# Kernel tuning notes

Hardware: AMD Instinct MI355X
Metric: run time of the kernel (lower is better)

The kernel has to match this reference:

```python
import jax, jax.numpy as jnp
import numpy as np

B, T, V = 8, 2048, 1024


def setup_inputs() -> dict:
    key = jax.random.key(0)
    k1, k2, k3, k4, k5 = jax.random.split(key, 5)
    idx = jax.random.randint(k1, (B, T), 0, V)
    # nn.Embedding(length, 1) weight, std=0.02
    v = 0.02 * jax.random.normal(k2, (T, 1), dtype=jnp.float32)
    # nn.Linear(V, V, bias=False) weights (torch layout: out x in), std=0.02
    Wk = 0.02 * jax.random.normal(k3, (V, V), dtype=jnp.float32)
    Wq = 0.02 * jax.random.normal(k4, (V, V), dtype=jnp.float32)
    Wv = 0.02 * jax.random.normal(k5, (V, V), dtype=jnp.float32)
    return {"idx": idx, "v": v, "Wk": Wk, "Wq": Wq, "Wv": Wv}


def reference(idx, v, Wk, Wq, Wv):
    Tn = v.shape[0]
    Vn = Wk.shape[0]
    # one-hot token embedding [B, T, V]
    e = jax.nn.one_hot(idx, Vn, dtype=jnp.float32)
    # relative positions, clipped at 0; pos_embd[i, j] = v[i-j] for i >= j else 0
    pos = jnp.arange(Tn)
    rel = jnp.clip(pos[:, None] - pos[None, :], 0)
    pos_embd = jnp.tril(v[rel, 0])  # [T, T]
    # layer_one = pos_embd @ e  -> [B, T, V]
    layer_one = jnp.einsum('ts,bsv->btv', pos_embd, e)
    K = layer_one @ Wk.T           # Linear: x @ W^T
    Q = e @ Wq.T
    attention = jnp.einsum('btv,bsv->bts', Q, K)  # [B, T, T]
    causal = jnp.tril(jnp.ones((Tn, Tn), dtype=bool))
    masked_attention = jnp.where(causal, attention, 0.0)
    output = jnp.einsum('bts,bsv->btv', masked_attention, e @ Wv.T)
    logits = output + 0.001
    return logits
```

## Files before the change

### kernel.cpp

```cpp
#include <hip/hip_runtime.h>
#include <stdint.h>

#define T_DIM 2048
#define V_DIM 1024
#define B_DIM 8
#define NT 16

typedef unsigned int u32;
typedef unsigned short u16;
typedef __attribute__((ext_vector_type(8))) short s16x8;
typedef __attribute__((ext_vector_type(4))) float f32x4;

__device__ __forceinline__ u16 f2bf(float x) {
  u32 u = __builtin_bit_cast(u32, x);
  u = u + 0x7FFFu + ((u >> 16) & 1u);
  return (u16)(u >> 16);
}

#define GLD16(gp, lp) __builtin_amdgcn_global_load_lds( \
    (const __attribute__((address_space(1))) u32*)(gp), \
    (__attribute__((address_space(3))) u32*)(lp), 16, 0, 0)

template<int MODE, bool F32OUT>
__global__ void __launch_bounds__(256, 2)
gemm_bt(const u16* __restrict__ A, int lda, long long batchA,
        const u16* __restrict__ Bt, int ldb, long long batchB,
        void* __restrict__ Cv, int ldc, long long batchC,
        int K, float bias)
{
  int bn, bm, bz;
  if (MODE == 0) {
    bn = blockIdx.x; bm = blockIdx.y; bz = blockIdx.z;
  } else if (MODE == 1) {
    int lam = blockIdx.x;
    int tau = lam >> 3; bz = lam & 7;
    int b = NT - 1, off = 0;
    while (tau >= off + (NT - b)) { off += NT - b; b--; }
    bn = b; bm = b + (tau - off);
  } else {
    int lam = blockIdx.x;
    bm = (NT - 1) - (lam >> 6);
    bn = (lam >> 3) & 7;
    bz = lam & 7;
  }
  const u16* Ab = A + (long long)bz * batchA;
  const u16* Bb = Bt + (long long)bz * batchB;
  int m0 = bm * 128, n0 = bn * 128;
  int kmax = K;
  if (MODE == 1) { int kl = (bn + 1) * 128; kmax = kl < K ? kl : K; }
  if (MODE == 2) { int kl = (bm + 1) * 128; kmax = kl < K ? kl : K; }

  __shared__ u16 As[128 * 64];
  __shared__ u16 Bs[128 * 64];

  int tid = threadIdx.x;
  int lane = tid & 63;
  int wid = tid >> 6;
  int wm = wid >> 1, wn = wid & 1;

  f32x4 acc[4][4] = {};

  int r0 = tid >> 3;
  int gcol = (((tid & 7) - r0) & 7) * 8;
  const u16* ga = Ab + (long long)(m0 + r0) * lda + gcol;
  const u16* gb = Bb + (long long)(n0 + r0) * ldb + gcol;
  u16* la = As + tid * 8;
  u16* lb = Bs + tid * 8;
  long long lda32 = (long long)32 * lda;
  long long ldb32 = (long long)32 * ldb;

  int rm = lane & 15;
  int q = lane >> 4;

  for (int k0 = 0; k0 < kmax; k0 += 64) {
#pragma unroll
    for (int i = 0; i < 4; i++)
      GLD16(ga + k0 + i * lda32, la + i * 2048);
#pragma unroll
    for (int i = 0; i < 4; i++)
      GLD16(gb + k0 + i * ldb32, lb + i * 2048);
    __syncthreads();
#pragma unroll
    for (int ks = 0; ks < 2; ks++) {
      s16x8 af[4], bfv[4];
#pragma unroll
      for (int mi = 0; mi < 4; mi++) {
        int row = wm * 64 + mi * 16 + rm;
        int p = ((ks * 4 + q) + row) & 7;
        af[mi] = *(const s16x8*)&As[row * 64 + p * 8];
      }
#pragma unroll
      for (int ni = 0; ni < 4; ni++) {
        int row = wn * 64 + ni * 16 + rm;
        int p = ((ks * 4 + q) + row) & 7;
        bfv[ni] = *(const s16x8*)&Bs[row * 64 + p * 8];
      }
#pragma unroll
      for (int mi = 0; mi < 4; mi++)
#pragma unroll
        for (int ni = 0; ni < 4; ni++)
          acc[mi][ni] = __builtin_amdgcn_mfma_f32_16x16x32_bf16(
              af[mi], bfv[ni], acc[mi][ni], 0, 0, 0);
    }
    __syncthreads();
  }

  int col = lane & 15;
  int rq = (lane >> 4) * 4;
#pragma unroll
  for (int mi = 0; mi < 4; mi++) {
#pragma unroll
    for (int ni = 0; ni < 4; ni++) {
      int lr = wm * 64 + mi * 16 + rq;
      int lc = wn * 64 + ni * 16 + col;
#pragma unroll
      for (int rr = 0; rr < 4; rr++) {
        float val = acc[mi][ni][rr];
        if (MODE == 1 && (n0 + lc) > (m0 + lr + rr)) val = 0.f;
        long long off = (long long)(m0 + lr + rr) * ldc + (n0 + lc);
        if (F32OUT) {
          float* C = (float*)Cv + (long long)bz * batchC;
          C[off] = val + bias;
        } else {
          u16* C = (u16*)Cv + (long long)bz * batchC;
          C[off] = f2bf(val);
        }
      }
    }
  }
}

__global__ void prep_weights(const float* __restrict__ Wq, u16* __restrict__ WqT,
                             const float* __restrict__ Wk, u16* __restrict__ WkT,
                             const float* __restrict__ Wv, u16* __restrict__ Wvb)
{
  int z = blockIdx.z;
  if (z == 2) {
    int bx = blockIdx.y * 32 + blockIdx.x;
    int i = bx * 1024 + threadIdx.y * 32 + threadIdx.x;
#pragma unroll
    for (int k = 0; k < 4; k++) Wvb[i + k * 256] = f2bf(Wv[i + k * 256]);
    return;
  }
  const float* src = z ? Wk : Wq;
  u16* dst = z ? WkT : WqT;
  __shared__ float tile[32][33];
  int x0 = blockIdx.x * 32, y0 = blockIdx.y * 32;
  int tx = threadIdx.x, ty = threadIdx.y;
#pragma unroll
  for (int k = 0; k < 4; k++)
    tile[ty + k * 8][tx] = src[(long long)(y0 + ty + k * 8) * V_DIM + x0 + tx];
  __syncthreads();
#pragma unroll
  for (int k = 0; k < 4; k++)
    dst[(long long)(x0 + ty + k * 8) * V_DIM + y0 + tx] = f2bf(tile[tx][ty + k * 8]);
}

__global__ void build_p(const float* __restrict__ v, u16* __restrict__ P)
{
  int gid = blockIdx.x * 256 + threadIdx.x;
  int e0 = gid * 8;
  int s = e0 >> 11, u0 = e0 & 2047;
  s16x8 o;
#pragma unroll
  for (int k = 0; k < 8; k++) {
    int u = u0 + k;
    o[k] = (short)((u <= s) ? f2bf(v[s - u]) : (u16)0);
  }
  *(s16x8*)&P[e0] = o;
}

__global__ void __launch_bounds__(256)
gather_gy(const int* __restrict__ idx, const u16* __restrict__ Mb,
          const u16* __restrict__ Wvb, u16* __restrict__ G,
          u16* __restrict__ Yt, int b0)
{
  int bx = blockIdx.x, z = blockIdx.y;
  const int* idxrow = idx + (long long)(b0 + z) * T_DIM;
  __shared__ u16 Row[V_DIM];
  int tid = threadIdx.x;
  const u32* src;
  u16* dst;
  if (bx < T_DIM) {
    src = (const u32*)(Mb + (long long)idxrow[bx] * V_DIM);
    dst = G + ((long long)z * T_DIM + bx) * T_DIM;
  } else {
    src = (const u32*)(Wvb + (long long)(bx - T_DIM) * V_DIM);
    dst = Yt + ((long long)z * V_DIM + (bx - T_DIM)) * T_DIM;
  }
  u32* dstl = (u32*)Row;
  dstl[tid] = src[tid];
  dstl[tid + 256] = src[tid + 256];
  __syncthreads();
  int s0 = tid * 8;
  int4 i0 = *(const int4*)&idxrow[s0];
  int4 i1 = *(const int4*)&idxrow[s0 + 4];
  s16x8 o;
  o[0] = (short)Row[i0.x]; o[1] = (short)Row[i0.y];
  o[2] = (short)Row[i0.z]; o[3] = (short)Row[i0.w];
  o[4] = (short)Row[i1.x]; o[5] = (short)Row[i1.y];
  o[6] = (short)Row[i1.z]; o[7] = (short)Row[i1.w];
  *(s16x8*)&dst[s0] = o;
}

extern "C" void kernel_launch(void* const* d_in, const int* in_sizes, int n_in,
                              void* d_out, int out_size, void* d_ws, size_t ws_size,
                              hipStream_t stream)
{
  const int*   idx = (const int*)d_in[0];
  const float* v   = (const float*)d_in[1];
  const float* Wk  = (const float*)d_in[2];
  const float* Wq  = (const float*)d_in[3];
  const float* Wv  = (const float*)d_in[4];
  float* out = (float*)d_out;

  char* p = (char*)d_ws;
  const size_t SZ_VV = (size_t)V_DIM * V_DIM * 2;
  const size_t SZ_TT = (size_t)T_DIM * T_DIM * 2;
  const size_t SZ_VT = (size_t)V_DIM * T_DIM * 2;
  u16* WqT = (u16*)p; p += SZ_VV;
  u16* WkT = (u16*)p; p += SZ_VV;
  u16* Wvb = (u16*)p; p += SZ_VV;
  u16* Mb  = (u16*)p; p += SZ_VV;
  u16* P   = (u16*)p; p += SZ_TT;
  size_t used = (size_t)(p - (char*)d_ws);
  size_t per = 2 * SZ_TT + SZ_VT;
  int nb = 8;
  while (nb > 1 && used + (size_t)nb * per > ws_size) nb >>= 1;
  u16* G    = (u16*)p; p += (size_t)nb * SZ_TT;
  u16* Abuf = (u16*)p; p += (size_t)nb * SZ_TT;
  u16* Yt   = (u16*)p;

  prep_weights<<<dim3(32, 32, 3), dim3(32, 8), 0, stream>>>(Wq, WqT, Wk, WkT, Wv, Wvb);
  build_p<<<2048, 256, 0, stream>>>(v, P);
  gemm_bt<0, false><<<dim3(V_DIM / 128, V_DIM / 128, 1), 256, 0, stream>>>(
      WqT, V_DIM, 0, WkT, V_DIM, 0, Mb, V_DIM, 0, V_DIM, 0.f);

  for (int b0 = 0; b0 < B_DIM; b0 += nb) {
    gather_gy<<<dim3(T_DIM + V_DIM, nb), 256, 0, stream>>>(idx, Mb, Wvb, G, Yt, b0);
    gemm_bt<1, false><<<dim3(nb * 136, 1, 1), 256, 0, stream>>>(
        G, T_DIM, (long long)T_DIM * T_DIM, P, T_DIM, 0,
        Abuf, T_DIM, (long long)T_DIM * T_DIM, T_DIM, 0.f);
    gemm_bt<2, true><<<dim3((V_DIM / 128) * nb * NT, 1, 1), 256, 0, stream>>>(
        Abuf, T_DIM, (long long)T_DIM * T_DIM, Yt, T_DIM, (long long)V_DIM * T_DIM,
        out + (long long)b0 * T_DIM * V_DIM, V_DIM, (long long)T_DIM * V_DIM,
        T_DIM, 0.001f);
  }
}
```

Measured before the change: 208.6 us.

## Replace batched GEMMs with 128x256-tile triple-buffered pipelined kernel

Adds a new GEMM kernel with 512 threads and 128x256 output tiles that triple-buffers LDS and splits prefetch loads across two compute phases using explicit vmcnt waits, barriers and setprio. Both the causal G·P GEMM and the A·Y output GEMM now use it, with a new triangular tile schedule over 256-wide column blocks. The goal is to hide global-load latency behind MFMA work and reuse each loaded A tile across twice as many columns. In exchange, the causal GEMM computes more wasted upper-triangle work per tile, LDS use and barrier count per k-step both rise, and the code relies on precise hand-placed waitcnt sequencing.

Result: faster. 203.9 us (-2.2%).

```diff
diff --git a/kernel.cpp b/kernel.cpp
--- a/kernel.cpp
+++ b/kernel.cpp
@@ -124,6 +124,186 @@
         } else {
           u16* C = (u16*)Cv + (long long)bz * batchC;
           C[off] = f2bf(val);
+        }
+      }
+    }
+  }
+}
+
+#define LDSB 24576
+#define FENCE() asm volatile("" ::: "memory")
+
+template<int MODE>
+__global__ void __launch_bounds__(512, 2)
+gemm8(const u16* __restrict__ Ag, int lda, long long batchA,
+      const u16* __restrict__ Btg, int ldb, long long batchB,
+      void* __restrict__ Cv, int ldc, long long batchC,
+      float bias, int lnb)
+{
+  int lam = blockIdx.x;
+  int bz = lam & ((1 << lnb) - 1);
+  int tau = lam >> lnb;
+  int m, n;
+  if (MODE == 1) {
+    int nn = 7, off = 0;
+    while (tau >= off + (16 - 2 * nn)) { off += 16 - 2 * nn; nn--; }
+    n = nn; m = 2 * nn + (tau - off);
+  } else {
+    m = 15 - (tau >> 2);
+    n = tau & 3;
+  }
+  const int m0 = m * 128, n0 = n * 256;
+  const int nk = (MODE == 1) ? (n + 1) * 4 : (m + 1) * 2;
+
+  const u16* __restrict__ Ab = Ag + (long long)bz * batchA;
+  const u16* __restrict__ Bb = Btg + (long long)bz * batchB;
+
+  __shared__ u16 lds[3 * LDSB];
+
+  const int tid = threadIdx.x;
+  const int lane = tid & 63;
+  const int wid = tid >> 6;
+  const int wm = wid >> 2, wn = wid & 3;
+
+  const u16* ga[2]; int la_[2];
+#pragma unroll
+  for (int i = 0; i < 2; i++) {
+    int f = i * 512 + tid, r = f >> 3, c = ((f & 7) - r) & 7;
+    ga[i] = Ab + (long long)(m0 + r) * lda + c * 8;
+    la_[i] = f * 8;
+  }
+  const u16* gb[4]; int lb_[4];
+#pragma unroll
+  for (int i = 0; i < 4; i++) {
+    int f = i * 512 + tid, r = f >> 3, c = ((f & 7) - r) & 7;
+    gb[i] = Bb + (long long)(n0 + r) * ldb + c * 8;
+    lb_[i] = 8192 + f * 8;
+  }
+
+  const int rm = lane & 15, q = lane >> 4;
+  int aoff[4][2], boff[4][2];
+#pragma unroll
+  for (int mi = 0; mi < 4; mi++)
+#pragma unroll
+    for (int ks = 0; ks < 2; ks++) {
+      int row = wm * 64 + mi * 16 + rm;
+      aoff[mi][ks] = row * 64 + (((ks * 4 + q) + row) & 7) * 8;
+    }
+#pragma unroll
+  for (int ni = 0; ni < 4; ni++)
+#pragma unroll
+    for (int ks = 0; ks < 2; ks++) {
+      int row = wn * 64 + ni * 16 + rm;
+      boff[ni][ks] = 8192 + row * 64 + (((ks * 4 + q) + row) & 7) * 8;
+    }
+
+  f32x4 acc[4][4] = {};
+
+#pragma unroll
+  for (int i = 0; i < 2; i++) GLD16(ga[i], &lds[la_[i]]);
+#pragma unroll
+  for (int i = 0; i < 4; i++) GLD16(gb[i], &lds[lb_[i]]);
+#pragma unroll
+  for (int i = 0; i < 2; i++) GLD16(ga[i] + 64, &lds[LDSB + la_[i]]);
+#pragma unroll
+  for (int i = 0; i < 4; i++) GLD16(gb[i] + 64, &lds[LDSB + lb_[i]]);
+
+  int cb = 0;
+  for (int kt = 0; kt < nk; ++kt) {
+    if (kt + 1 < nk) asm volatile("s_waitcnt vmcnt(6)" ::: "memory");
+    else             asm volatile("s_waitcnt vmcnt(0)" ::: "memory");
+    __builtin_amdgcn_s_barrier();
+    FENCE();
+
+    const u16* Abuf = &lds[cb];
+    int pb = cb + 2 * LDSB; if (pb >= 3 * LDSB) pb -= 3 * LDSB;
+    const bool pf = (kt + 2) < nk;
+    const int pk = (kt + 2) * 64;
+
+    s16x8 af[4][2], bf0[2][2];
+#pragma unroll
+    for (int mi = 0; mi < 4; mi++)
+#pragma unroll
+      for (int ks = 0; ks < 2; ks++)
+        af[mi][ks] = *(const s16x8*)&Abuf[aoff[mi][ks]];
+#pragma unroll
+    for (int ni = 0; ni < 2; ni++)
+#pragma unroll
+      for (int ks = 0; ks < 2; ks++)
+        bf0[ni][ks] = *(const s16x8*)&Abuf[boff[ni][ks]];
+    if (pf) {
+      GLD16(ga[0] + pk, &lds[pb + la_[0]]);
+      GLD16(ga[1] + pk, &lds[pb + la_[1]]);
+      GLD16(gb[0] + pk, &lds[pb + lb_[0]]);
+    }
+    __builtin_amdgcn_s_barrier();
+    FENCE();
+    __builtin_amdgcn_s_setprio(1);
+#pragma unroll
+    for (int ks = 0; ks < 2; ks++)
+#pragma unroll
+      for (int mi = 0; mi < 4; mi++)
+#pragma unroll
+        for (int ni = 0; ni < 2; ni++)
+          acc[mi][ni] = __builtin_amdgcn_mfma_f32_16x16x32_bf16(
+              af[mi][ks], bf0[ni][ks], acc[mi][ni], 0, 0, 0);
+    __builtin_amdgcn_s_setprio(0);
+    __builtin_amdgcn_s_barrier();
+    FENCE();
+
+    s16x8 bf1[2][2];
+#pragma unroll
+    for (int ni = 0; ni < 2; ni++)
+#pragma unroll
+      for (int ks = 0; ks < 2; ks++)
+        bf1[ni][ks] = *(const s16x8*)&Abuf[boff[ni + 2][ks]];
+    if (pf) {
+      GLD16(gb[1] + pk, &lds[pb + lb_[1]]);
+      GLD16(gb[2] + pk, &lds[pb + lb_[2]]);
+      GLD16(gb[3] + pk, &lds[pb + lb_[3]]);
+    }
+    __builtin_amdgcn_s_barrier();
+    FENCE();
+    __builtin_amdgcn_s_setprio(1);
+#pragma unroll
+    for (int ks = 0; ks < 2; ks++)
+#pragma unroll
+      for (int mi = 0; mi < 4; mi++)
+#pragma unroll
+        for (int ni = 0; ni < 2; ni++)
+          acc[mi][ni + 2] = __builtin_amdgcn_mfma_f32_16x16x32_bf16(
+              af[mi][ks], bf1[ni][ks], acc[mi][ni + 2], 0, 0, 0);
+    __builtin_amdgcn_s_setprio(0);
+    cb += LDSB; if (cb >= 3 * LDSB) cb = 0;
+  }
+
+  const int col = lane & 15, rq = (lane >> 4) * 4;
+  if (MODE == 2) {
+    float* C = (float*)Cv + (long long)bz * batchC;
+#pragma unroll
+    for (int mi = 0; mi < 4; mi++) {
+      int lr = m0 + wm * 64 + mi * 16 + rq;
+#pragma unroll
+      for (int ni = 0; ni < 4; ni++) {
+        int lc = n0 + wn * 64 + ni * 16 + col;
+#pragma unroll
+        for (int rr = 0; rr < 4; rr++)
+          C[(long long)(lr + rr) * ldc + lc] = acc[mi][ni][rr] + bias;
+      }
+    }
+  } else {
+    u16* C = (u16*)Cv + (long long)bz * batchC;
+#pragma unroll
+    for (int mi = 0; mi < 4; mi++) {
+      int lr = m0 + wm * 64 + mi * 16 + rq;
+#pragma unroll
+      for (int ni = 0; ni < 4; ni++) {
+        int lc = n0 + wn * 64 + ni * 16 + col;
+#pragma unroll
+        for (int rr = 0; rr < 4; rr++) {
+          float val = acc[mi][ni][rr];
+          if (lc > lr + rr) val = 0.f;
+          C[(long long)(lr + rr) * ldc + lc] = f2bf(val);
         }
       }
     }
@@ -230,6 +410,7 @@
   u16* G    = (u16*)p; p += (size_t)nb * SZ_TT;
   u16* Abuf = (u16*)p; p += (size_t)nb * SZ_TT;
   u16* Yt   = (u16*)p;
+  int lnb = (nb == 8) ? 3 : (nb == 4) ? 2 : (nb == 2) ? 1 : 0;
 
   prep_weights<<<dim3(32, 32, 3), dim3(32, 8), 0, stream>>>(Wq, WqT, Wk, WkT, Wv, Wvb);
   build_p<<<2048, 256, 0, stream>>>(v, P);
@@ -238,12 +419,12 @@
 
   for (int b0 = 0; b0 < B_DIM; b0 += nb) {
     gather_gy<<<dim3(T_DIM + V_DIM, nb), 256, 0, stream>>>(idx, Mb, Wvb, G, Yt, b0);
-    gemm_bt<1, false><<<dim3(nb * 136, 1, 1), 256, 0, stream>>>(
+    gemm8<1><<<dim3(72 * nb), 512, 0, stream>>>(
         G, T_DIM, (long long)T_DIM * T_DIM, P, T_DIM, 0,
-        Abuf, T_DIM, (long long)T_DIM * T_DIM, T_DIM, 0.f);
-    gemm_bt<2, true><<<dim3((V_DIM / 128) * nb * NT, 1, 1), 256, 0, stream>>>(
+        Abuf, T_DIM, (long long)T_DIM * T_DIM, 0.f, lnb);
+    gemm8<2><<<dim3(64 * nb), 512, 0, stream>>>(
         Abuf, T_DIM, (long long)T_DIM * T_DIM, Yt, T_DIM, (long long)V_DIM * T_DIM,
         out + (long long)b0 * T_DIM * V_DIM, V_DIM, (long long)T_DIM * V_DIM,
-        T_DIM, 0.001f);
-  }
-}
+        0.001f, lnb);
+  }
+}
```

## Replace batched triangular GEMMs with 256x256-tile double-buffered pipelined kernel

Applied to the files above, without the earlier changes.

Adds a new gemm8 kernel for the two large batched GEMMs. It uses 512-thread blocks computing 256x256 tiles with 8 waves, two LDS buffers, and explicit interleaving of global-to-LDS prefetch, LDS reads and MFMA groups. These are controlled by manual waitcnt, barriers and setprio. The triangular tile scheduling and K-limit skipping are kept at the coarser 256 granularity, and gemm_bt is simplified to the plain mode only. The goal is more data reuse per tile and hiding load latency behind MFMA work, at the cost of coarser triangular work skipping and higher register and LDS pressure.

New measurement: 279.2 us. 33.9% more time.

```diff
diff --git a/kernel.cpp b/kernel.cpp
--- a/kernel.cpp
+++ b/kernel.cpp
@@ -4,7 +4,6 @@
 #define T_DIM 2048
 #define V_DIM 1024
 #define B_DIM 8
-#define NT 16
 
 typedef unsigned int u32;
 typedef unsigned short u16;
@@ -28,27 +27,11 @@
         void* __restrict__ Cv, int ldc, long long batchC,
         int K, float bias)
 {
-  int bn, bm, bz;
-  if (MODE == 0) {
-    bn = blockIdx.x; bm = blockIdx.y; bz = blockIdx.z;
-  } else if (MODE == 1) {
-    int lam = blockIdx.x;
-    int tau = lam >> 3; bz = lam & 7;
-    int b = NT - 1, off = 0;
-    while (tau >= off + (NT - b)) { off += NT - b; b--; }
-    bn = b; bm = b + (tau - off);
-  } else {
-    int lam = blockIdx.x;
-    bm = (NT - 1) - (lam >> 6);
-    bn = (lam >> 3) & 7;
-    bz = lam & 7;
-  }
+  int bn = blockIdx.x, bm = blockIdx.y, bz = blockIdx.z;
   const u16* Ab = A + (long long)bz * batchA;
   const u16* Bb = Bt + (long long)bz * batchB;
   int m0 = bm * 128, n0 = bn * 128;
   int kmax = K;
-  if (MODE == 1) { int kl = (bn + 1) * 128; kmax = kl < K ? kl : K; }
-  if (MODE == 2) { int kl = (bm + 1) * 128; kmax = kl < K ? kl : K; }
 
   __shared__ u16 As[128 * 64];
   __shared__ u16 Bs[128 * 64];
@@ -116,7 +99,6 @@
 #pragma unroll
       for (int rr = 0; rr < 4; rr++) {
         float val = acc[mi][ni][rr];
-        if (MODE == 1 && (n0 + lc) > (m0 + lr + rr)) val = 0.f;
         long long off = (long long)(m0 + lr + rr) * ldc + (n0 + lc);
         if (F32OUT) {
           float* C = (float*)Cv + (long long)bz * batchC;
@@ -124,6 +106,166 @@
         } else {
           u16* C = (u16*)Cv + (long long)bz * batchC;
           C[off] = f2bf(val);
+        }
+      }
+    }
+  }
+}
+
+#define BUFE 32768
+
+#define STAGE_A(h, bb, kt) { \
+  GLD16(gA[h][0] + (kt) * 64, &lds[(bb) + lA[h][0]]); \
+  GLD16(gA[h][1] + (kt) * 64, &lds[(bb) + lA[h][1]]); }
+#define STAGE_B(h, bb, kt) { \
+  GLD16(gB[h][0] + (kt) * 64, &lds[(bb) + lB[h][0]]); \
+  GLD16(gB[h][1] + (kt) * 64, &lds[(bb) + lB[h][1]]); }
+
+#define DS_A(quad, ksv, bb) { \
+  _Pragma("unroll") \
+  for (int mi = 0; mi < 4; mi++) \
+    af[mi] = *(const s16x8*)&lds[(bb) + abase[ksv] + ((quad) * 4 + mi) * 1024]; }
+#define DS_B(ksv, bb) { \
+  _Pragma("unroll") \
+  for (int ni = 0; ni < 4; ni++) \
+    bf[ni] = *(const s16x8*)&lds[(bb) + bbase[ksv] + ni * 1024]; }
+
+#define MFMA16(quad) { \
+  __builtin_amdgcn_s_setprio(1); \
+  _Pragma("unroll") \
+  for (int mi = 0; mi < 4; mi++) \
+    _Pragma("unroll") \
+    for (int ni = 0; ni < 4; ni++) \
+      acc[(quad) * 4 + mi][ni] = __builtin_amdgcn_mfma_f32_16x16x32_bf16( \
+          af[mi], bf[ni], acc[(quad) * 4 + mi][ni], 0, 0, 0); \
+  __builtin_amdgcn_s_setprio(0); }
+
+#define BARS() { __builtin_amdgcn_s_barrier(); __builtin_amdgcn_sched_barrier(0); }
+#define LGKM0() { asm volatile("s_waitcnt lgkmcnt(0)" ::: "memory"); \
+                  __builtin_amdgcn_sched_barrier(0); }
+#define VMC(n) asm volatile("s_waitcnt vmcnt(" #n ")" ::: "memory")
+
+template<int MODE>
+__global__ void __launch_bounds__(512, 2)
+gemm8(const u16* __restrict__ Ag, int lda, long long batchA,
+      const u16* __restrict__ Btg, int ldb, long long batchB,
+      void* __restrict__ Cv, int ldc, long long batchC,
+      float bias, int lnb)
+{
+  int lam = blockIdx.x;
+  int bz = lam & ((1 << lnb) - 1);
+  int tau = lam >> lnb;
+  int m, n;
+  if (MODE == 1) {
+    int nn = 7, off = 0;
+    while (tau >= off + (8 - nn)) { off += 8 - nn; nn--; }
+    n = nn; m = nn + (tau - off);
+  } else {
+    m = 7 - (tau >> 2);
+    n = tau & 3;
+  }
+  const int m0 = m * 256, n0 = n * 256;
+  const int nk = ((MODE == 1 ? n : m) + 1) * 4;
+
+  const u16* __restrict__ Ab = Ag + (long long)bz * batchA;
+  const u16* __restrict__ Bb = Btg + (long long)bz * batchB;
+
+  __shared__ u16 lds[2 * BUFE];
+
+  const int tid = threadIdx.x;
+  const int lane = tid & 63;
+  const int wid = tid >> 6;
+  const int wm = wid >> 2, wn = wid & 3;
+
+  const u16 *gA[2][2], *gB[2][2];
+  int lA[2][2], lB[2][2];
+#pragma unroll
+  for (int h = 0; h < 2; h++)
+#pragma unroll
+    for (int l = 0; l < 2; l++) {
+      int f = l * 512 + tid, r = f >> 3, c = ((f & 7) - r) & 7;
+      gA[h][l] = Ab + (long long)(m0 + h * 128 + r) * lda + c * 8;
+      gB[h][l] = Bb + (long long)(n0 + h * 128 + r) * ldb + c * 8;
+      lA[h][l] = h * 8192 + f * 8;
+      lB[h][l] = 16384 + h * 8192 + f * 8;
+    }
+
+  const int rm = lane & 15, q = lane >> 4;
+  int abase[2], bbase[2];
+#pragma unroll
+  for (int ks = 0; ks < 2; ks++) {
+    abase[ks] = wm * 8192 + rm * 64 + (((ks * 4 + q) + rm) & 7) * 8;
+    bbase[ks] = 16384 + (wn >> 1) * 8192 + ((wn & 1) * 64 + rm) * 64
+              + (((ks * 4 + q) + rm) & 7) * 8;
+  }
+
+  f32x4 acc[8][4] = {};
+
+  STAGE_A(0, 0, 0); STAGE_B(0, 0, 0); STAGE_B(1, 0, 0); STAGE_A(1, 0, 0);
+  STAGE_A(0, BUFE, 1); STAGE_B(0, BUFE, 1); STAGE_B(1, BUFE, 1);
+  VMC(6);
+  __builtin_amdgcn_s_barrier();
+  __builtin_amdgcn_sched_barrier(0);
+
+  const int niter = nk >> 1;
+  for (int j = 0; j < niter; ++j) {
+    const int ktY = 2 * j + 1;
+    const int pk = 2 * j + 2;
+    const bool pf = pk < nk;
+    s16x8 af[4], bf[4];
+
+    DS_A(0, 0, 0); DS_B(0, 0);
+    STAGE_A(1, BUFE, ktY);
+    BARS(); LGKM0(); MFMA16(0); BARS();
+    DS_A(1, 0, 0);
+    BARS(); LGKM0(); MFMA16(1); BARS();
+    DS_A(0, 1, 0); DS_B(1, 0);
+    BARS(); LGKM0(); MFMA16(0); BARS();
+    DS_A(1, 1, 0);
+    if (pf) { STAGE_A(0, 0, pk); STAGE_B(0, 0, pk); VMC(4); }
+    else    { VMC(0); }
+    BARS(); LGKM0(); MFMA16(1); BARS();
+    DS_A(0, 0, BUFE); DS_B(0, BUFE);
+    if (pf) { STAGE_B(1, 0, pk); STAGE_A(1, 0, pk); }
+    BARS(); LGKM0(); MFMA16(0); BARS();
+    DS_A(1, 0, BUFE);
+    BARS(); LGKM0(); MFMA16(1); BARS();
+    DS_A(0, 1, BUFE); DS_B(1, BUFE);
+    BARS(); LGKM0(); MFMA16(0); BARS();
+    DS_A(1, 1, BUFE);
+    if (pf) { STAGE_A(0, BUFE, pk + 1); STAGE_B(0, BUFE, pk + 1);
+              STAGE_B(1, BUFE, pk + 1); VMC(6); }
+    else    { VMC(0); }
+    BARS(); LGKM0(); MFMA16(1); BARS();
+  }
+
+  const int col = lane & 15, rq = (lane >> 4) * 4;
+  if (MODE == 2) {
+    float* C = (float*)Cv + (long long)bz * batchC;
+#pragma unroll
+    for (int mi = 0; mi < 8; mi++) {
+      int lr = m0 + wm * 128 + mi * 16 + rq;
+#pragma unroll
+      for (int ni = 0; ni < 4; ni++) {
+        int lc = n0 + wn * 64 + ni * 16 + col;
+#pragma unroll
+        for (int rr = 0; rr < 4; rr++)
+          C[(long long)(lr + rr) * ldc + lc] = acc[mi][ni][rr] + bias;
+      }
+    }
+  } else {
+    u16* C = (u16*)Cv + (long long)bz * batchC;
+#pragma unroll
+    for (int mi = 0; mi < 8; mi++) {
+      int lr = m0 + wm * 128 + mi * 16 + rq;
+#pragma unroll
+      for (int ni = 0; ni < 4; ni++) {
+        int lc = n0 + wn * 64 + ni * 16 + col;
+#pragma unroll
+        for (int rr = 0; rr < 4; rr++) {
+          float val = acc[mi][ni][rr];
+          if (lc > lr + rr) val = 0.f;
+          C[(long long)(lr + rr) * ldc + lc] = f2bf(val);
         }
       }
     }
@@ -230,6 +372,7 @@
   u16* G    = (u16*)p; p += (size_t)nb * SZ_TT;
   u16* Abuf = (u16*)p; p += (size_t)nb * SZ_TT;
   u16* Yt   = (u16*)p;
+  int lnb = (nb == 8) ? 3 : (nb == 4) ? 2 : (nb == 2) ? 1 : 0;
 
   prep_weights<<<dim3(32, 32, 3), dim3(32, 8), 0, stream>>>(Wq, WqT, Wk, WkT, Wv, Wvb);
   build_p<<<2048, 256, 0, stream>>>(v, P);
@@ -238,12 +381,12 @@
 
   for (int b0 = 0; b0 < B_DIM; b0 += nb) {
     gather_gy<<<dim3(T_DIM + V_DIM, nb), 256, 0, stream>>>(idx, Mb, Wvb, G, Yt, b0);
-    gemm_bt<1, false><<<dim3(nb * 136, 1, 1), 256, 0, stream>>>(
+    gemm8<1><<<dim3(36 * nb), 512, 0, stream>>>(
         G, T_DIM, (long long)T_DIM * T_DIM, P, T_DIM, 0,
-        Abuf, T_DIM, (long long)T_DIM * T_DIM, T_DIM, 0.f);
-    gemm_bt<2, true><<<dim3((V_DIM / 128) * nb * NT, 1, 1), 256, 0, stream>>>(
+        Abuf, T_DIM, (long long)T_DIM * T_DIM, 0.f, lnb);
+    gemm8<2><<<dim3(32 * nb), 512, 0, stream>>>(
         Abuf, T_DIM, (long long)T_DIM * T_DIM, Yt, T_DIM, (long long)V_DIM * T_DIM,
         out + (long long)b0 * T_DIM * V_DIM, V_DIM, (long long)T_DIM * V_DIM,
-        T_DIM, 0.001f);
-  }
-}
+        0.001f, lnb);
+  }
+}
```

## Double-buffer A tiles, load B fragments directly to registers, skip unused triangle writes

Applied to the files above, without the earlier changes.

The batched GEMMs now double-buffer the A tile in LDS and prefetch the next stage while computing the current one. They use manual vmcnt waits and raw barriers, and load B operand fragments straight from global memory into registers instead of staging them through LDS. build_p and gather_gy also skip writing elements beyond the 128-aligned causal limit that the triangular GEMMs never read. The aim is to hide global latency and cut LDS traffic and write bandwidth. The risks are uncoalesced B register loads and the correctness of the hand-written wait counts.

New measurement: 274.1 us. 1.31x slower.

```diff
diff --git a/kernel.cpp b/kernel.cpp
--- a/kernel.cpp
+++ b/kernel.cpp
@@ -8,6 +8,7 @@
 
 typedef unsigned int u32;
 typedef unsigned short u16;
+typedef long long ll;
 typedef __attribute__((ext_vector_type(8))) short s16x8;
 typedef __attribute__((ext_vector_type(4))) float f32x4;
 
@@ -21,17 +22,91 @@
     (const __attribute__((address_space(1))) u32*)(gp), \
     (__attribute__((address_space(3))) u32*)(lp), 16, 0, 0)
 
-template<int MODE, bool F32OUT>
+#define VMC(n) asm volatile("s_waitcnt vmcnt(" #n ")" ::: "memory")
+#define BARF() { asm volatile("" ::: "memory"); \
+                 __builtin_amdgcn_s_barrier(); \
+                 asm volatile("" ::: "memory"); }
+
 __global__ void __launch_bounds__(256, 2)
-gemm_bt(const u16* __restrict__ A, int lda, long long batchA,
-        const u16* __restrict__ Bt, int ldb, long long batchB,
-        void* __restrict__ Cv, int ldc, long long batchC,
-        int K, float bias)
+gemm_vv(const u16* __restrict__ A, const u16* __restrict__ Bt, u16* __restrict__ C)
+{
+  int bn = blockIdx.x, bm = blockIdx.y;
+  int m0 = bm * 128, n0 = bn * 128;
+
+  __shared__ u16 As[128 * 64];
+  __shared__ u16 Bs[128 * 64];
+
+  int tid = threadIdx.x;
+  int lane = tid & 63;
+  int wid = tid >> 6;
+  int wm = wid >> 1, wn = wid & 1;
+
+  f32x4 acc[4][4] = {};
+
+  int r0 = tid >> 3;
+  int gcol = (((tid & 7) - r0) & 7) * 8;
+  const u16* ga = A + (ll)(m0 + r0) * V_DIM + gcol;
+  const u16* gb = Bt + (ll)(n0 + r0) * V_DIM + gcol;
+  u16* la = As + tid * 8;
+  u16* lb = Bs + tid * 8;
+  const ll ld32 = (ll)32 * V_DIM;
+
+  int rm = lane & 15;
+  int q = lane >> 4;
+
+  for (int k0 = 0; k0 < V_DIM; k0 += 64) {
+#pragma unroll
+    for (int i = 0; i < 4; i++) GLD16(ga + k0 + i * ld32, la + i * 2048);
+#pragma unroll
+    for (int i = 0; i < 4; i++) GLD16(gb + k0 + i * ld32, lb + i * 2048);
+    __syncthreads();
+#pragma unroll
+    for (int ks = 0; ks < 2; ks++) {
+      s16x8 af[4], bfv[4];
+#pragma unroll
+      for (int mi = 0; mi < 4; mi++) {
+        int row = wm * 64 + mi * 16 + rm;
+        int p = ((ks * 4 + q) + row) & 7;
+        af[mi] = *(const s16x8*)&As[row * 64 + p * 8];
+      }
+#pragma unroll
+      for (int ni = 0; ni < 4; ni++) {
+        int row = wn * 64 + ni * 16 + rm;
+        int p = ((ks * 4 + q) + row) & 7;
+        bfv[ni] = *(const s16x8*)&Bs[row * 64 + p * 8];
+      }
+#pragma unroll
+      for (int mi = 0; mi < 4; mi++)
+#pragma unroll
+        for (int ni = 0; ni < 4; ni++)
+          acc[mi][ni] = __builtin_amdgcn_mfma_f32_16x16x32_bf16(
+              af[mi], bfv[ni], acc[mi][ni], 0, 0, 0);
+    }
+    __syncthreads();
+  }
+
+  int col = lane & 15;
+  int rq = (lane >> 4) * 4;
+#pragma unroll
+  for (int mi = 0; mi < 4; mi++)
+#pragma unroll
+    for (int ni = 0; ni < 4; ni++) {
+      int lr = wm * 64 + mi * 16 + rq;
+      int lc = wn * 64 + ni * 16 + col;
+#pragma unroll
+      for (int rr = 0; rr < 4; rr++)
+        C[(ll)(m0 + lr + rr) * V_DIM + (n0 + lc)] = f2bf(acc[mi][ni][rr]);
+    }
+}
+
+template<int MODE>
+__global__ void __launch_bounds__(256, 2)
+gemm_br(const u16* __restrict__ Ag, int lda, ll batchA,
+        const u16* __restrict__ Btg, int ldb, ll batchB,
+        void* __restrict__ Cv, int ldc, ll batchC, float bias)
 {
   int bn, bm, bz;
-  if (MODE == 0) {
-    bn = blockIdx.x; bm = blockIdx.y; bz = blockIdx.z;
-  } else if (MODE == 1) {
+  if (MODE == 1) {
     int lam = blockIdx.x;
     int tau = lam >> 3; bz = lam & 7;
     int b = NT - 1, off = 0;
@@ -43,70 +118,71 @@
     bn = (lam >> 3) & 7;
     bz = lam & 7;
   }
-  const u16* Ab = A + (long long)bz * batchA;
-  const u16* Bb = Bt + (long long)bz * batchB;
-  int m0 = bm * 128, n0 = bn * 128;
-  int kmax = K;
-  if (MODE == 1) { int kl = (bn + 1) * 128; kmax = kl < K ? kl : K; }
-  if (MODE == 2) { int kl = (bm + 1) * 128; kmax = kl < K ? kl : K; }
-
-  __shared__ u16 As[128 * 64];
-  __shared__ u16 Bs[128 * 64];
-
-  int tid = threadIdx.x;
-  int lane = tid & 63;
-  int wid = tid >> 6;
-  int wm = wid >> 1, wn = wid & 1;
-
-  f32x4 acc[4][4] = {};
+  const u16* __restrict__ Ab = Ag + (ll)bz * batchA;
+  const u16* __restrict__ Bb = Btg + (ll)bz * batchB;
+  const int m0 = bm * 128, n0 = bn * 128;
+  const int kmax = ((MODE == 1 ? bn : bm) + 1) * 128;
+  const int nkt = kmax >> 6;
+
+  __shared__ u16 As[2][128 * 64];
+
+  const int tid = threadIdx.x;
+  const int lane = tid & 63;
+  const int wid = tid >> 6;
+  const int wm = wid >> 1, wn = wid & 1;
+  const int rm = lane & 15, q = lane >> 4;
 
   int r0 = tid >> 3;
   int gcol = (((tid & 7) - r0) & 7) * 8;
-  const u16* ga = Ab + (long long)(m0 + r0) * lda + gcol;
-  const u16* gb = Bb + (long long)(n0 + r0) * ldb + gcol;
-  u16* la = As + tid * 8;
-  u16* lb = Bs + tid * 8;
-  long long lda32 = (long long)32 * lda;
-  long long ldb32 = (long long)32 * ldb;
-
-  int rm = lane & 15;
-  int q = lane >> 4;
-
-  for (int k0 = 0; k0 < kmax; k0 += 64) {
-#pragma unroll
-    for (int i = 0; i < 4; i++)
-      GLD16(ga + k0 + i * lda32, la + i * 2048);
-#pragma unroll
-    for (int i = 0; i < 4; i++)
-      GLD16(gb + k0 + i * ldb32, lb + i * 2048);
-    __syncthreads();
-#pragma unroll
-    for (int ks = 0; ks < 2; ks++) {
-      s16x8 af[4], bfv[4];
-#pragma unroll
-      for (int mi = 0; mi < 4; mi++) {
-        int row = wm * 64 + mi * 16 + rm;
-        int p = ((ks * 4 + q) + row) & 7;
-        af[mi] = *(const s16x8*)&As[row * 64 + p * 8];
-      }
-#pragma unroll
-      for (int ni = 0; ni < 4; ni++) {
-        int row = wn * 64 + ni * 16 + rm;
-        int p = ((ks * 4 + q) + row) & 7;
-        bfv[ni] = *(const s16x8*)&Bs[row * 64 + p * 8];
-      }
-#pragma unroll
-      for (int mi = 0; mi < 4; mi++)
-#pragma unroll
-        for (int ni = 0; ni < 4; ni++)
-          acc[mi][ni] = __builtin_amdgcn_mfma_f32_16x16x32_bf16(
-              af[mi], bfv[ni], acc[mi][ni], 0, 0, 0);
-    }
-    __syncthreads();
-  }
-
-  int col = lane & 15;
-  int rq = (lane >> 4) * 4;
+  const u16* ga = Ab + (ll)(m0 + r0) * lda + gcol;
+  const ll lda32 = (ll)32 * lda;
+
+  const u16* gbn[4];
+#pragma unroll
+  for (int ni = 0; ni < 4; ni++)
+    gbn[ni] = Bb + (ll)(n0 + wn * 64 + ni * 16 + rm) * ldb + q * 8;
+
+  f32x4 acc[4][4] = {};
+  s16x8 b0[2][4], b1[2][4];
+
+#define STAGEA(buf, kt) { \
+  _Pragma("unroll") for (int i = 0; i < 4; i++) \
+    GLD16(ga + (kt) * 64 + i * lda32, &As[buf][0] + tid * 8 + i * 2048); }
+
+#define LOADB(dst, kt) { \
+  _Pragma("unroll") for (int ks = 0; ks < 2; ks++) \
+    _Pragma("unroll") for (int ni = 0; ni < 4; ni++) \
+      dst[ks][ni] = *(const s16x8*)(gbn[ni] + (kt) * 64 + ks * 32); }
+
+#define COMPUTE(buf, bv) { \
+  _Pragma("unroll") for (int ks = 0; ks < 2; ks++) { \
+    s16x8 af[4]; \
+    _Pragma("unroll") for (int mi = 0; mi < 4; mi++) { \
+      int row = wm * 64 + mi * 16 + rm; \
+      int p = ((ks * 4 + q) + row) & 7; \
+      af[mi] = *(const s16x8*)&As[buf][row * 64 + p * 8]; \
+    } \
+    _Pragma("unroll") for (int mi = 0; mi < 4; mi++) \
+      _Pragma("unroll") for (int ni = 0; ni < 4; ni++) \
+        acc[mi][ni] = __builtin_amdgcn_mfma_f32_16x16x32_bf16( \
+            af[mi], bv[ks][ni], acc[mi][ni], 0, 0, 0); \
+  } }
+
+  STAGEA(0, 0); LOADB(b0, 0);
+  __syncthreads();
+
+  for (int kt = 0; kt < nkt; kt += 2) {
+    STAGEA(1, kt + 1); LOADB(b1, kt + 1);
+    COMPUTE(0, b0);
+    VMC(8);
+    BARF();
+    const bool more = (kt + 2 < nkt);
+    if (more) { STAGEA(0, kt + 2); LOADB(b0, kt + 2); }
+    COMPUTE(1, b1);
+    if (more) { VMC(8); BARF(); }
+  }
+
+  const int col = lane & 15, rq = (lane >> 4) * 4;
 #pragma unroll
   for (int mi = 0; mi < 4; mi++) {
 #pragma unroll
@@ -117,17 +193,20 @@
       for (int rr = 0; rr < 4; rr++) {
         float val = acc[mi][ni][rr];
         if (MODE == 1 && (n0 + lc) > (m0 + lr + rr)) val = 0.f;
-        long long off = (long long)(m0 + lr + rr) * ldc + (n0 + lc);
-        if (F32OUT) {
-          float* C = (float*)Cv + (long long)bz * batchC;
+        ll off = (ll)(m0 + lr + rr) * ldc + (n0 + lc);
+        if (MODE == 2) {
+          float* C = (float*)Cv + (ll)bz * batchC;
           C[off] = val + bias;
         } else {
-          u16* C = (u16*)Cv + (long long)bz * batchC;
+          u16* C = (u16*)Cv + (ll)bz * batchC;
           C[off] = f2bf(val);
         }
       }
     }
   }
+#undef STAGEA
+#undef LOADB
+#undef COMPUTE
 }
 
 __global__ void prep_weights(const float* __restrict__ Wq, u16* __restrict__ WqT,
@@ -149,11 +228,11 @@
   int tx = threadIdx.x, ty = threadIdx.y;
 #pragma unroll
   for (int k = 0; k < 4; k++)
-    tile[ty + k * 8][tx] = src[(long long)(y0 + ty + k * 8) * V_DIM + x0 + tx];
+    tile[ty + k * 8][tx] = src[(ll)(y0 + ty + k * 8) * V_DIM + x0 + tx];
   __syncthreads();
 #pragma unroll
   for (int k = 0; k < 4; k++)
-    dst[(long long)(x0 + ty + k * 8) * V_DIM + y0 + tx] = f2bf(tile[tx][ty + k * 8]);
+    dst[(ll)(x0 + ty + k * 8) * V_DIM + y0 + tx] = f2bf(tile[tx][ty + k * 8]);
 }
 
 __global__ void build_p(const float* __restrict__ v, u16* __restrict__ P)
@@ -161,6 +240,8 @@
   int gid = blockIdx.x * 256 + threadIdx.x;
   int e0 = gid * 8;
   int s = e0 >> 11, u0 = e0 & 2047;
+  int lim = ((s >> 7) + 1) << 7;
+  if (u0 >= lim) return;
   s16x8 o;
 #pragma unroll
   for (int k = 0; k < 8; k++) {
@@ -176,23 +257,26 @@
           u16* __restrict__ Yt, int b0)
 {
   int bx = blockIdx.x, z = blockIdx.y;
-  const int* idxrow = idx + (long long)(b0 + z) * T_DIM;
+  const int* idxrow = idx + (ll)(b0 + z) * T_DIM;
   __shared__ u16 Row[V_DIM];
   int tid = threadIdx.x;
   const u32* src;
   u16* dst;
+  int lim = T_DIM;
   if (bx < T_DIM) {
-    src = (const u32*)(Mb + (long long)idxrow[bx] * V_DIM);
-    dst = G + ((long long)z * T_DIM + bx) * T_DIM;
+    src = (const u32*)(Mb + (ll)idxrow[bx] * V_DIM);
+    dst = G + ((ll)z * T_DIM + bx) * T_DIM;
+    lim = ((bx >> 7) + 1) << 7;
   } else {
-    src = (const u32*)(Wvb + (long long)(bx - T_DIM) * V_DIM);
-    dst = Yt + ((long long)z * V_DIM + (bx - T_DIM)) * T_DIM;
+    src = (const u32*)(Wvb + (ll)(bx - T_DIM) * V_DIM);
+    dst = Yt + ((ll)z * V_DIM + (bx - T_DIM)) * T_DIM;
   }
   u32* dstl = (u32*)Row;
   dstl[tid] = src[tid];
   dstl[tid + 256] = src[tid + 256];
   __syncthreads();
   int s0 = tid * 8;
+  if (s0 >= lim) return;
   int4 i0 = *(const int4*)&idxrow[s0];
   int4 i1 = *(const int4*)&idxrow[s0 + 4];
   s16x8 o;
@@ -233,17 +317,16 @@
 
   prep_weights<<<dim3(32, 32, 3), dim3(32, 8), 0, stream>>>(Wq, WqT, Wk, WkT, Wv, Wvb);
   build_p<<<2048, 256, 0, stream>>>(v, P);
-  gemm_bt<0, false><<<dim3(V_DIM / 128, V_DIM / 128, 1), 256, 0, stream>>>(
-      WqT, V_DIM, 0, WkT, V_DIM, 0, Mb, V_DIM, 0, V_DIM, 0.f);
+  gemm_vv<<<dim3(V_DIM / 128, V_DIM / 128, 1), 256, 0, stream>>>(WqT, WkT, Mb);
 
   for (int b0 = 0; b0 < B_DIM; b0 += nb) {
     gather_gy<<<dim3(T_DIM + V_DIM, nb), 256, 0, stream>>>(idx, Mb, Wvb, G, Yt, b0);
-    gemm_bt<1, false><<<dim3(nb * 136, 1, 1), 256, 0, stream>>>(
-        G, T_DIM, (long long)T_DIM * T_DIM, P, T_DIM, 0,
-        Abuf, T_DIM, (long long)T_DIM * T_DIM, T_DIM, 0.f);
-    gemm_bt<2, true><<<dim3((V_DIM / 128) * nb * NT, 1, 1), 256, 0, stream>>>(
-        Abuf, T_DIM, (long long)T_DIM * T_DIM, Yt, T_DIM, (long long)V_DIM * T_DIM,
-        out + (long long)b0 * T_DIM * V_DIM, V_DIM, (long long)T_DIM * V_DIM,
-        T_DIM, 0.001f);
-  }
-}
+    gemm_br<1><<<dim3(nb * 136, 1, 1), 256, 0, stream>>>(
+        G, T_DIM, (ll)T_DIM * T_DIM, P, T_DIM, 0,
+        Abuf, T_DIM, (ll)T_DIM * T_DIM, 0.f);
+    gemm_br<2><<<dim3((V_DIM / 128) * nb * NT, 1, 1), 256, 0, stream>>>(
+        Abuf, T_DIM, (ll)T_DIM * T_DIM, Yt, T_DIM, (ll)V_DIM * T_DIM,
+        out + (ll)b0 * T_DIM * V_DIM, V_DIM, (ll)T_DIM * V_DIM,
+        0.001f);
+  }
+}
```
